# Kernel optimization log

Hardware: AMD Instinct MI355X
Metric: run time of the kernel (lower is better)

Reference implementation:

```python
import jax, jax.numpy as jnp
import numpy as np

NUM_HEADS = 16
HEAD_DIM = 64
D_DEC = 1024
D_ENC = 1024
R = 256  # kv_lora_rank
LN_EPS = 1e-5


def setup_inputs() -> dict:
    key = jax.random.key(0)
    ks = jax.random.split(key, 8)
    B, SQ, SK = 4, 2048, 4096
    query = jax.random.normal(ks[0], (B, SQ, D_DEC), dtype=jnp.float32)
    encoder_output = jax.random.normal(ks[1], (B, SK, D_ENC), dtype=jnp.float32)
    s = 0.02
    Wq = jax.random.normal(ks[2], (NUM_HEADS * HEAD_DIM, D_DEC), dtype=jnp.float32) * s
    Wkva = jax.random.normal(ks[3], (R, D_ENC), dtype=jnp.float32) * s
    ln_g = jnp.ones((R,), dtype=jnp.float32)
    ln_b = jnp.zeros((R,), dtype=jnp.float32)
    Wkvb = jax.random.normal(ks[4], (NUM_HEADS * 2 * HEAD_DIM, R), dtype=jnp.float32) * s
    Wout = jax.random.normal(ks[5], (D_DEC, NUM_HEADS * HEAD_DIM), dtype=jnp.float32) * s
    return {"query": query, "encoder_output": encoder_output, "Wq": Wq,
            "Wkva": Wkva, "ln_g": ln_g, "ln_b": ln_b, "Wkvb": Wkvb, "Wout": Wout}


def reference(query, encoder_output, Wq, Wkva, ln_g, ln_b, Wkvb, Wout):
    B, SQ, _ = query.shape
    SK = encoder_output.shape[1]
    H, Dh = NUM_HEADS, HEAD_DIM

    # q projection -> [B, H, SQ, Dh]
    q = jnp.einsum('bsd,ed->bse', query, Wq).reshape(B, SQ, H, Dh).transpose(0, 2, 1, 3)

    # low-rank KV compression + layernorm
    c = jnp.einsum('bsd,rd->bsr', encoder_output, Wkva)  # [B, SK, R]
    mu = jnp.mean(c, axis=-1, keepdims=True)
    var = jnp.mean(jnp.square(c - mu), axis=-1, keepdims=True)
    c = (c - mu) * jax.lax.rsqrt(var + LN_EPS) * ln_g + ln_b

    # decompress to K,V: [B, SK, H, 2*Dh] -> split
    kv = jnp.einsum('bsr,er->bse', c, Wkvb).reshape(B, SK, H, 2 * Dh).transpose(0, 2, 1, 3)
    k, v = kv[..., :Dh], kv[..., Dh:]

    scale = 1.0 / np.sqrt(Dh).astype(np.float32)
    scores = jnp.einsum('bhqd,bhkd->bhqk', q, k) * scale
    attn = jax.nn.softmax(scores, axis=-1)  # dropout is identity in eval / p=0
    o = jnp.einsum('bhqk,bhkd->bhqd', attn, v)
    o = o.transpose(0, 2, 1, 3).reshape(B, SQ, H * Dh)
    return jnp.einsum('bse,de->bsd', o, Wout)
```

## Files before the change

### kernel.cpp

```cpp
#include <hip/hip_runtime.h>

#define LOG2E 1.4426950408889634f

typedef __attribute__((ext_vector_type(8))) short short8;
typedef __attribute__((ext_vector_type(4))) float f32x4;
typedef __attribute__((ext_vector_type(16))) float f32x16;
typedef __attribute__((ext_vector_type(4))) unsigned u32x4;

__device__ inline unsigned short f2bf(float f) {
  unsigned u = __float_as_uint(f);
  u += 0x7fffu + ((u >> 16) & 1u);
  return (unsigned short)(u >> 16);
}

#define MFMA16(a, b, c) __builtin_amdgcn_mfma_f32_16x16x32_bf16((a), (b), (c), 0, 0, 0)
#define MFMA32(a, b, c) __builtin_amdgcn_mfma_f32_32x32x16_bf16((a), (b), (c), 0, 0, 0)

#define GLDS16(gp, lp)                                                              \
  __builtin_amdgcn_global_load_lds((const __attribute__((address_space(1))) void*)(gp), \
                                   (__attribute__((address_space(3))) void*)(lp), 16, 0, 0)

__device__ inline f32x4 zero4() {
  f32x4 z = {0.f, 0.f, 0.f, 0.f};
  return z;
}
__device__ inline f32x16 zero16() {
  f32x16 z = {0.f, 0.f, 0.f, 0.f, 0.f, 0.f, 0.f, 0.f, 0.f, 0.f, 0.f, 0.f, 0.f, 0.f, 0.f, 0.f};
  return z;
}
__device__ inline unsigned cvtpk_bf16(float a, float b) {
  unsigned r;
  asm("v_cvt_pk_bf16_f32 %0, %1, %2" : "=v"(r) : "v"(a), "v"(b));
  return r;
}
__device__ inline void plswap(unsigned& a, unsigned& b) {
  asm("v_permlane32_swap_b32 %0, %1" : "+v"(a), "+v"(b));
}

__global__ __launch_bounds__(256) void k_cast6(
    const float* __restrict__ e, const float* __restrict__ q, const float* __restrict__ wq,
    const float* __restrict__ wo, const float* __restrict__ wb, const float* __restrict__ wa,
    unsigned short* __restrict__ eo, unsigned short* __restrict__ qo, unsigned short* __restrict__ wqo,
    unsigned short* __restrict__ woo, unsigned short* __restrict__ wbo, unsigned short* __restrict__ wao) {
  int i = (blockIdx.x * 256 + threadIdx.x) * 4;
  const float* src;
  unsigned short* dst;
  int off;
  if (i < 16777216) { src = e; dst = eo; off = i; }
  else if (i < 25165824) { src = q; dst = qo; off = i - 16777216; }
  else if (i < 26214400) { src = wq; dst = wqo; off = i - 25165824; }
  else if (i < 27262976) { src = wo; dst = woo; off = i - 26214400; }
  else if (i < 27787264) { src = wb; dst = wbo; off = i - 27262976; }
  else { src = wa; dst = wao; off = i - 27787264; }
  float4 v = *(const float4*)(src + off);
  unsigned lo = (unsigned)f2bf(v.x) | ((unsigned)f2bf(v.y) << 16);
  unsigned hi = (unsigned)f2bf(v.z) | ((unsigned)f2bf(v.w) << 16);
  *(uint2*)(dst + off) = make_uint2(lo, hi);
}

__global__ __launch_bounds__(256, 2) void k_qproj(const unsigned short* __restrict__ A,
                                                  const unsigned short* __restrict__ Bw,
                                                  unsigned short* __restrict__ Qout) {
  __shared__ __align__(16) short As[128 * 32];
  __shared__ __align__(16) short Bs[128 * 32];
  const int K = 1024;
  int tid = threadIdx.x;
  int w = tid >> 6, lane = tid & 63, quad = lane >> 4, c = lane & 15;
  int m0 = blockIdx.x * 128, n0 = blockIdx.y * 128;
  int wm = (w >> 1) * 64, wn = (w & 1) * 64;
  f32x4 acc[4][4];
#pragma unroll
  for (int i = 0; i < 4; i++)
#pragma unroll
    for (int j = 0; j < 4; j++) acc[i][j] = zero4();

  for (int k0 = 0; k0 < K; k0 += 32) {
#pragma unroll
    for (int i = 0; i < 2; i++) {
      int seg = w * 2 + i;
      int bo = seg * 1024 + lane * 16;
      int row = bo >> 6, col = (bo & 63) >> 1;
      GLDS16(A + (size_t)(m0 + row) * K + k0 + col, (char*)As + seg * 1024);
      GLDS16(Bw + (size_t)(n0 + row) * K + k0 + col, (char*)Bs + seg * 1024);
    }
    __syncthreads();
    short8 af[4], bfr[4];
#pragma unroll
    for (int i = 0; i < 4; i++) {
      af[i] = *(const short8*)&As[(wm + i * 16 + c) * 32 + quad * 8];
      bfr[i] = *(const short8*)&Bs[(wn + i * 16 + c) * 32 + quad * 8];
    }
#pragma unroll
    for (int mi = 0; mi < 4; mi++)
#pragma unroll
      for (int ni = 0; ni < 4; ni++) acc[mi][ni] = MFMA16(af[mi], bfr[ni], acc[mi][ni]);
    __syncthreads();
  }
  const float scale = 0.125f * LOG2E;
#pragma unroll
  for (int mi = 0; mi < 4; mi++) {
    int rowb = m0 + wm + mi * 16 + quad * 4;
#pragma unroll
    for (int ni = 0; ni < 4; ni++) {
      int col = n0 + wn + ni * 16 + c;
      int h = col >> 6, d = col & 63;
#pragma unroll
      for (int r = 0; r < 4; r++) {
        int row = rowb + r;
        int b = row >> 11, sq = row & 2047;
        Qout[(((size_t)(b * 16 + h)) * 2048 + sq) * 64 + d] = f2bf(acc[mi][ni][r] * scale);
      }
    }
  }
}

__global__ __launch_bounds__(256, 2) void k_cln(const unsigned short* __restrict__ E,
                                                const unsigned short* __restrict__ Wa,
                                                const float* __restrict__ g, const float* __restrict__ bb,
                                                unsigned short* __restrict__ Cout) {
  __shared__ __align__(16) short As[64 * 32];
  __shared__ __align__(16) short Bs[256 * 32];
  __shared__ float redS[4][64], redQ[4][64];
  __shared__ float gS[256], bS[256];
  const int K = 1024;
  int tid = threadIdx.x;
  int w = tid >> 6, lane = tid & 63, quad = lane >> 4, c = lane & 15;
  int m0 = blockIdx.x * 64;
  gS[tid] = g[tid];
  bS[tid] = bb[tid];
  f32x4 acc[4][4];
#pragma unroll
  for (int i = 0; i < 4; i++)
#pragma unroll
    for (int j = 0; j < 4; j++) acc[i][j] = zero4();

  for (int k0 = 0; k0 < K; k0 += 32) {
    {
      int bo = w * 1024 + lane * 16;
      int row = bo >> 6, col = (bo & 63) >> 1;
      GLDS16(E + (size_t)(m0 + row) * K + k0 + col, (char*)As + w * 1024);
    }
#pragma unroll
    for (int i = 0; i < 4; i++) {
      int seg = w * 4 + i;
      int bo = seg * 1024 + lane * 16;
      int row = bo >> 6, col = (bo & 63) >> 1;
      GLDS16(Wa + (size_t)row * K + k0 + col, (char*)Bs + seg * 1024);
    }
    __syncthreads();
    short8 af[4], bfr[4];
#pragma unroll
    for (int i = 0; i < 4; i++) {
      af[i] = *(const short8*)&As[(i * 16 + c) * 32 + quad * 8];
      bfr[i] = *(const short8*)&Bs[(w * 64 + i * 16 + c) * 32 + quad * 8];
    }
#pragma unroll
    for (int mi = 0; mi < 4; mi++)
#pragma unroll
      for (int ni = 0; ni < 4; ni++) acc[mi][ni] = MFMA16(af[mi], bfr[ni], acc[mi][ni]);
    __syncthreads();
  }
  float ps[4][4], pq[4][4];
#pragma unroll
  for (int mi = 0; mi < 4; mi++)
#pragma unroll
    for (int r = 0; r < 4; r++) {
      float s = 0.f, q = 0.f;
#pragma unroll
      for (int ni = 0; ni < 4; ni++) {
        float x = acc[mi][ni][r];
        s += x;
        q += x * x;
      }
      for (int m = 1; m < 16; m <<= 1) {
        s += __shfl_xor(s, m, 64);
        q += __shfl_xor(q, m, 64);
      }
      ps[mi][r] = s;
      pq[mi][r] = q;
    }
  if (c == 0) {
#pragma unroll
    for (int mi = 0; mi < 4; mi++)
#pragma unroll
      for (int r = 0; r < 4; r++) {
        int row = mi * 16 + quad * 4 + r;
        redS[w][row] = ps[mi][r];
        redQ[w][row] = pq[mi][r];
      }
  }
  __syncthreads();
  float muv[4][4], rsv[4][4];
#pragma unroll
  for (int mi = 0; mi < 4; mi++)
#pragma unroll
    for (int r = 0; r < 4; r++) {
      int row = mi * 16 + quad * 4 + r;
      float S = redS[0][row] + redS[1][row] + redS[2][row] + redS[3][row];
      float Q = redQ[0][row] + redQ[1][row] + redQ[2][row] + redQ[3][row];
      float mu = S * (1.f / 256.f);
      float var = Q * (1.f / 256.f) - mu * mu;
      muv[mi][r] = mu;
      rsv[mi][r] = rsqrtf(var + 1e-5f);
    }
#pragma unroll
  for (int mi = 0; mi < 4; mi++)
#pragma unroll
    for (int ni = 0; ni < 4; ni++) {
      int col = w * 64 + ni * 16 + c;
#pragma unroll
      for (int r = 0; r < 4; r++) {
        int row = m0 + mi * 16 + quad * 4 + r;
        float y = (acc[mi][ni][r] - muv[mi][r]) * rsv[mi][r] * gS[col] + bS[col];
        Cout[(size_t)row * 256 + col] = f2bf(y);
      }
    }
}

__global__ __launch_bounds__(256, 2) void k_kv(const unsigned short* __restrict__ A,
                                               const unsigned short* __restrict__ Bw,
                                               unsigned short* __restrict__ Kb,
                                               unsigned short* __restrict__ Vb) {
  __shared__ __align__(16) short As[128 * 32];
  __shared__ __align__(16) short Bs[128 * 32];
  const int K = 256;
  int tid = threadIdx.x;
  int w = tid >> 6, lane = tid & 63, quad = lane >> 4, c = lane & 15;
  int m0 = blockIdx.x * 128, n0 = blockIdx.y * 128;
  int wm = (w >> 1) * 64, wn = (w & 1) * 64;
  f32x4 acc[4][4];
#pragma unroll
  for (int i = 0; i < 4; i++)
#pragma unroll
    for (int j = 0; j < 4; j++) acc[i][j] = zero4();

  for (int k0 = 0; k0 < K; k0 += 32) {
#pragma unroll
    for (int i = 0; i < 2; i++) {
      int seg = w * 2 + i;
      int bo = seg * 1024 + lane * 16;
      int row = bo >> 6, col = (bo & 63) >> 1;
      GLDS16(A + (size_t)(m0 + row) * K + k0 + col, (char*)As + seg * 1024);
      GLDS16(Bw + (size_t)(n0 + row) * K + k0 + col, (char*)Bs + seg * 1024);
    }
    __syncthreads();
    short8 af[4], bfr[4];
#pragma unroll
    for (int i = 0; i < 4; i++) {
      af[i] = *(const short8*)&As[(wm + i * 16 + c) * 32 + quad * 8];
      bfr[i] = *(const short8*)&Bs[(wn + i * 16 + c) * 32 + quad * 8];
    }
#pragma unroll
    for (int mi = 0; mi < 4; mi++)
#pragma unroll
      for (int ni = 0; ni < 4; ni++) acc[mi][ni] = MFMA16(af[mi], bfr[ni], acc[mi][ni]);
    __syncthreads();
  }
#pragma unroll
  for (int mi = 0; mi < 4; mi++) {
    int rowb = m0 + wm + mi * 16 + quad * 4;
#pragma unroll
    for (int ni = 0; ni < 4; ni++) {
      int col = n0 + wn + ni * 16 + c;
      int h = col >> 7, rr = col & 127;
#pragma unroll
      for (int r = 0; r < 4; r++) {
        int row = rowb + r;
        int b = row >> 12, sk = row & 4095;
        int kt = sk >> 6, ki = sk & 63;
        size_t base = ((size_t)(b * 16 + h)) * 262144 + (size_t)kt * 4096;
        float x = acc[mi][ni][r];
        if (rr < 64) {
          int d = rr;
          int half = ki >> 5, l31k = ki & 31, ds = d >> 4, dhi = (d >> 3) & 1, j = d & 7;
          Kb[base + (size_t)((half * 4 + ds) * 64 + l31k + 32 * dhi) * 8 + j] = f2bf(x);
        } else {
          int d = rr - 64;
          int dt = d >> 5, sg = ki >> 4, khi = (ki >> 3) & 1, j = ki & 7;
          Vb[base + (size_t)((dt * 4 + sg) * 64 + (d & 31) + 32 * khi) * 8 + j] = f2bf(x);
        }
      }
    }
  }
}

__device__ __forceinline__ void attn_tile(const char* Kl, const char* Vl,
                                          const short8 (&qf)[4], f32x16 (&O)[2], float& lp) {
#pragma unroll
  for (int h = 0; h < 2; h++) {
    short8 kf[4];
#pragma unroll
    for (int ds = 0; ds < 4; ds++) kf[ds] = *(const short8*)(Kl + (h * 4 + ds) * 1024);
    f32x16 S = zero16();
#pragma unroll
    for (int ds = 0; ds < 4; ds++) S = MFMA32(kf[ds], qf[ds], S);
    float lpa = 0.f, lpb = 0.f;
    unsigned u[8];
#pragma unroll
    for (int m = 0; m < 8; m++) {
      float p0 = __builtin_amdgcn_exp2f(S[2 * m]);
      float p1 = __builtin_amdgcn_exp2f(S[2 * m + 1]);
      if (m & 1) lpb += p0 + p1; else lpa += p0 + p1;
      u[m] = cvtpk_bf16(p0, p1);
    }
    lp += lpa + lpb;
    plswap(u[0], u[2]);
    plswap(u[1], u[3]);
    plswap(u[4], u[6]);
    plswap(u[5], u[7]);
    u32x4 w0 = {u[0], u[1], u[2], u[3]};
    u32x4 w1 = {u[4], u[5], u[6], u[7]};
    short8 paf0 = __builtin_bit_cast(short8, w0);
    short8 paf1 = __builtin_bit_cast(short8, w1);
#pragma unroll
    for (int dt = 0; dt < 2; dt++) {
      short8 vf0 = *(const short8*)(Vl + (dt * 4 + h * 2 + 0) * 1024);
      short8 vf1 = *(const short8*)(Vl + (dt * 4 + h * 2 + 1) * 1024);
      O[dt] = MFMA32(paf0, vf0, O[dt]);
      O[dt] = MFMA32(paf1, vf1, O[dt]);
    }
  }
}

__global__ __launch_bounds__(256, 4) void k_attn(const unsigned short* __restrict__ Qb,
                                                 const unsigned short* __restrict__ Kb,
                                                 const unsigned short* __restrict__ Vb,
                                                 unsigned short* __restrict__ Ob) {
  __shared__ __align__(16) short KA[8192];
  __shared__ __align__(16) short KB[8192];
  int tid = threadIdx.x;
  int w = tid >> 6, lane = tid & 63;
  int l31 = lane & 31, hi = lane >> 5;
  int qt = blockIdx.x, bh = blockIdx.y;

  const char* Kg = (const char*)Kb + (size_t)bh * 524288;
  const char* Vg = (const char*)Vb + (size_t)bh * 524288;
  int ldsseg = (w < 2) ? w * 4 : 8 + (w - 2) * 4;
  const char* sgbase = ((w < 2) ? Kg + (w * 4) * 1024 : Vg + ((w - 2) * 4) * 1024) + lane * 16;

  const unsigned short* Qrow = Qb + ((size_t)bh * 2048 + qt * 128 + w * 32 + l31) * 64 + hi * 8;
  short8 qf[4];
#pragma unroll
  for (int ds = 0; ds < 4; ds++) qf[ds] = *(const short8*)(Qrow + ds * 16);

  f32x16 O[2];
  float lp = 0.f;
#pragma unroll
  for (int j = 0; j < 2; j++) O[j] = zero16();

#pragma unroll
  for (int i = 0; i < 4; i++) GLDS16(sgbase + i * 1024, (char*)KA + (ldsseg + i) * 1024);
  sgbase += 8192;
  __syncthreads();

  for (int kt2 = 0; kt2 < 64; kt2 += 2) {
    {
#pragma unroll
      for (int i = 0; i < 4; i++)
        GLDS16(sgbase + i * 1024, (char*)KB + (ldsseg + i) * 1024);
      sgbase += 8192;
      attn_tile((const char*)KA + lane * 16, (const char*)KA + lane * 16 + 8192, qf, O, lp);
      __syncthreads();
    }
    {
      if (kt2 < 62) {
#pragma unroll
        for (int i = 0; i < 4; i++)
          GLDS16(sgbase + i * 1024, (char*)KA + (ldsseg + i) * 1024);
        sgbase += 8192;
      }
      attn_tile((const char*)KB + lane * 16, (const char*)KB + lane * 16 + 8192, qf, O, lp);
      __syncthreads();
    }
  }

  lp += __shfl_xor(lp, 32, 64);
  int b = bh >> 4, hh = bh & 15;
#pragma unroll
  for (int r = 0; r < 16; r++) {
    int qrow = (r & 3) + 8 * (r >> 2) + 4 * hi;
    float inv = __builtin_amdgcn_rcpf(__shfl(lp, qrow, 64));
    size_t orow = ((size_t)b * 2048 + qt * 128 + w * 32 + qrow) * 1024 + hh * 64 + l31;
    Ob[orow] = f2bf(O[0][r] * inv);
    Ob[orow + 32] = f2bf(O[1][r] * inv);
  }
}

__global__ __launch_bounds__(256, 2) void k_out(const unsigned short* __restrict__ A,
                                                const unsigned short* __restrict__ Bw,
                                                float* __restrict__ Out) {
  __shared__ __align__(16) short As[128 * 32];
  __shared__ __align__(16) short Bs[128 * 32];
  const int K = 1024;
  int tid = threadIdx.x;
  int w = tid >> 6, lane = tid & 63, quad = lane >> 4, c = lane & 15;
  int m0 = blockIdx.x * 128, n0 = blockIdx.y * 128;
  int wm = (w >> 1) * 64, wn = (w & 1) * 64;
  f32x4 acc[4][4];
#pragma unroll
  for (int i = 0; i < 4; i++)
#pragma unroll
    for (int j = 0; j < 4; j++) acc[i][j] = zero4();

  for (int k0 = 0; k0 < K; k0 += 32) {
#pragma unroll
    for (int i = 0; i < 2; i++) {
      int seg = w * 2 + i;
      int bo = seg * 1024 + lane * 16;
      int row = bo >> 6, col = (bo & 63) >> 1;
      GLDS16(A + (size_t)(m0 + row) * K + k0 + col, (char*)As + seg * 1024);
      GLDS16(Bw + (size_t)(n0 + row) * K + k0 + col, (char*)Bs + seg * 1024);
    }
    __syncthreads();
    short8 af[4], bfr[4];
#pragma unroll
    for (int i = 0; i < 4; i++) {
      af[i] = *(const short8*)&As[(wm + i * 16 + c) * 32 + quad * 8];
      bfr[i] = *(const short8*)&Bs[(wn + i * 16 + c) * 32 + quad * 8];
    }
#pragma unroll
    for (int mi = 0; mi < 4; mi++)
#pragma unroll
      for (int ni = 0; ni < 4; ni++) acc[mi][ni] = MFMA16(af[mi], bfr[ni], acc[mi][ni]);
    __syncthreads();
  }
#pragma unroll
  for (int mi = 0; mi < 4; mi++) {
    int rowb = m0 + wm + mi * 16 + quad * 4;
#pragma unroll
    for (int ni = 0; ni < 4; ni++) {
      int col = n0 + wn + ni * 16 + c;
#pragma unroll
      for (int r = 0; r < 4; r++) Out[(size_t)(rowb + r) * 1024 + col] = acc[mi][ni][r];
    }
  }
}

extern "C" void kernel_launch(void* const* d_in, const int* in_sizes, int n_in,
                              void* d_out, int out_size, void* d_ws, size_t ws_size,
                              hipStream_t stream) {
  const float* query = (const float*)d_in[0];
  const float* enc = (const float*)d_in[1];
  const float* Wq = (const float*)d_in[2];
  const float* Wkva = (const float*)d_in[3];
  const float* ln_g = (const float*)d_in[4];
  const float* ln_b = (const float*)d_in[5];
  const float* Wkvb = (const float*)d_in[6];
  const float* Wout = (const float*)d_in[7];
  if (ws_size < 81264640) return;

  char* ws = (char*)d_ws;
  unsigned short* wq_bf = (unsigned short*)(ws + 0);
  unsigned short* wa_bf = (unsigned short*)(ws + 2097152);
  unsigned short* wb_bf = (unsigned short*)(ws + 2621440);
  unsigned short* wo_bf = (unsigned short*)(ws + 3670016);
  unsigned short* qproj = (unsigned short*)(ws + 5767168);
  unsigned short* cln = (unsigned short*)(ws + 22544384);
  unsigned short* ebf_v = (unsigned short*)(ws + 30932992);
  unsigned short* qin_o = (unsigned short*)(ws + 64487424);
  unsigned short* kbuf = (unsigned short*)d_out;

  k_cast6<<<27392, 256, 0, stream>>>(enc, query, Wq, Wout, Wkvb, Wkva,
                                     ebf_v, qin_o, wq_bf, wo_bf, wb_bf, wa_bf);

  k_qproj<<<dim3(64, 8), 256, 0, stream>>>(qin_o, wq_bf, qproj);
  k_cln<<<256, 256, 0, stream>>>(ebf_v, wa_bf, ln_g, ln_b, cln);
  k_kv<<<dim3(128, 16), 256, 0, stream>>>(cln, wb_bf, kbuf, ebf_v);
  k_attn<<<dim3(16, 64), 256, 0, stream>>>(qproj, kbuf, ebf_v, qin_o);
  k_out<<<dim3(64, 8), 256, 0, stream>>>(qin_o, wo_bf, (float*)d_out);
}
```

Baseline: 423.2 us.

## Fuse activation bf16 casts into GEMM loaders, vectorize V stores, prioritize MFMA

The separate cast kernel no longer converts the large encoder and query activations. The q-projection and compression GEMMs now read fp32 directly, convert to bf16 in registers and store into LDS, which removes a full write and re-read of the bf16 copies. The K/V epilogue is restructured to pack four bf16 V values per 8-byte store. In the attention inner loop, setprio is raised around the MFMA groups. The trade-off is that the GEMM A loads become synchronous register loads instead of async global-to-LDS loads, so that latency is exposed.

```diff
diff --git a/kernel.cpp b/kernel.cpp
--- a/kernel.cpp
+++ b/kernel.cpp
@@ -37,28 +37,26 @@
   asm("v_permlane32_swap_b32 %0, %1" : "+v"(a), "+v"(b));
 }
 
-__global__ __launch_bounds__(256) void k_cast6(
-    const float* __restrict__ e, const float* __restrict__ q, const float* __restrict__ wq,
-    const float* __restrict__ wo, const float* __restrict__ wb, const float* __restrict__ wa,
-    unsigned short* __restrict__ eo, unsigned short* __restrict__ qo, unsigned short* __restrict__ wqo,
-    unsigned short* __restrict__ woo, unsigned short* __restrict__ wbo, unsigned short* __restrict__ wao) {
+__global__ __launch_bounds__(256) void k_cast4(
+    const float* __restrict__ wq, const float* __restrict__ wo,
+    const float* __restrict__ wb, const float* __restrict__ wa,
+    unsigned short* __restrict__ wqo, unsigned short* __restrict__ woo,
+    unsigned short* __restrict__ wbo, unsigned short* __restrict__ wao) {
   int i = (blockIdx.x * 256 + threadIdx.x) * 4;
   const float* src;
   unsigned short* dst;
   int off;
-  if (i < 16777216) { src = e; dst = eo; off = i; }
-  else if (i < 25165824) { src = q; dst = qo; off = i - 16777216; }
-  else if (i < 26214400) { src = wq; dst = wqo; off = i - 25165824; }
-  else if (i < 27262976) { src = wo; dst = woo; off = i - 26214400; }
-  else if (i < 27787264) { src = wb; dst = wbo; off = i - 27262976; }
-  else { src = wa; dst = wao; off = i - 27787264; }
+  if (i < 1048576) { src = wq; dst = wqo; off = i; }
+  else if (i < 2097152) { src = wo; dst = woo; off = i - 1048576; }
+  else if (i < 2621440) { src = wb; dst = wbo; off = i - 2097152; }
+  else { src = wa; dst = wao; off = i - 2621440; }
   float4 v = *(const float4*)(src + off);
   unsigned lo = (unsigned)f2bf(v.x) | ((unsigned)f2bf(v.y) << 16);
   unsigned hi = (unsigned)f2bf(v.z) | ((unsigned)f2bf(v.w) << 16);
   *(uint2*)(dst + off) = make_uint2(lo, hi);
 }
 
-__global__ __launch_bounds__(256, 2) void k_qproj(const unsigned short* __restrict__ A,
+__global__ __launch_bounds__(256, 2) void k_qproj(const float* __restrict__ A,
                                                   const unsigned short* __restrict__ Bw,
                                                   unsigned short* __restrict__ Qout) {
   __shared__ __align__(16) short As[128 * 32];
@@ -68,6 +66,7 @@
   int w = tid >> 6, lane = tid & 63, quad = lane >> 4, c = lane & 15;
   int m0 = blockIdx.x * 128, n0 = blockIdx.y * 128;
   int wm = (w >> 1) * 64, wn = (w & 1) * 64;
+  int rsub = lane >> 2, csub = (lane & 3) * 8;
   f32x4 acc[4][4];
 #pragma unroll
   for (int i = 0; i < 4; i++)
@@ -75,12 +74,21 @@
     for (int j = 0; j < 4; j++) acc[i][j] = zero4();
 
   for (int k0 = 0; k0 < K; k0 += 32) {
+#pragma unroll
+    for (int i = 0; i < 2; i++) {
+      int seg = w * 2 + i;
+      const float* Ap = A + (size_t)(m0 + seg * 16 + rsub) * K + k0 + csub;
+      float4 va = *(const float4*)Ap;
+      float4 vb2 = *(const float4*)(Ap + 4);
+      u32x4 pk = {cvtpk_bf16(va.x, va.y), cvtpk_bf16(va.z, va.w),
+                  cvtpk_bf16(vb2.x, vb2.y), cvtpk_bf16(vb2.z, vb2.w)};
+      *(u32x4*)((char*)As + seg * 1024 + lane * 16) = pk;
+    }
 #pragma unroll
     for (int i = 0; i < 2; i++) {
       int seg = w * 2 + i;
       int bo = seg * 1024 + lane * 16;
       int row = bo >> 6, col = (bo & 63) >> 1;
-      GLDS16(A + (size_t)(m0 + row) * K + k0 + col, (char*)As + seg * 1024);
       GLDS16(Bw + (size_t)(n0 + row) * K + k0 + col, (char*)Bs + seg * 1024);
     }
     __syncthreads();
@@ -114,7 +122,7 @@
   }
 }
 
-__global__ __launch_bounds__(256, 2) void k_cln(const unsigned short* __restrict__ E,
+__global__ __launch_bounds__(256, 2) void k_cln(const float* __restrict__ E,
                                                 const unsigned short* __restrict__ Wa,
                                                 const float* __restrict__ g, const float* __restrict__ bb,
                                                 unsigned short* __restrict__ Cout) {
@@ -126,6 +134,7 @@
   int tid = threadIdx.x;
   int w = tid >> 6, lane = tid & 63, quad = lane >> 4, c = lane & 15;
   int m0 = blockIdx.x * 64;
+  int rsub = lane >> 2, csub = (lane & 3) * 8;
   gS[tid] = g[tid];
   bS[tid] = bb[tid];
   f32x4 acc[4][4];
@@ -136,9 +145,12 @@
 
   for (int k0 = 0; k0 < K; k0 += 32) {
     {
-      int bo = w * 1024 + lane * 16;
-      int row = bo >> 6, col = (bo & 63) >> 1;
-      GLDS16(E + (size_t)(m0 + row) * K + k0 + col, (char*)As + w * 1024);
+      const float* Ep = E + (size_t)(m0 + w * 16 + rsub) * K + k0 + csub;
+      float4 va = *(const float4*)Ep;
+      float4 vb2 = *(const float4*)(Ep + 4);
+      u32x4 pk = {cvtpk_bf16(va.x, va.y), cvtpk_bf16(va.z, va.w),
+                  cvtpk_bf16(vb2.x, vb2.y), cvtpk_bf16(vb2.z, vb2.w)};
+      *(u32x4*)((char*)As + w * 1024 + lane * 16) = pk;
     }
 #pragma unroll
     for (int i = 0; i < 4; i++) {
@@ -259,26 +271,33 @@
 #pragma unroll
   for (int mi = 0; mi < 4; mi++) {
     int rowb = m0 + wm + mi * 16 + quad * 4;
+    int b = rowb >> 12;
+    int sk0 = rowb & 4095;
+    int kt = sk0 >> 6, ki0 = sk0 & 63;
+    int sg = ((wm + mi * 16) & 63) >> 4;
+    int khi = quad >> 1;
+    int j0 = (quad & 1) * 4;
 #pragma unroll
     for (int ni = 0; ni < 4; ni++) {
       int col = n0 + wn + ni * 16 + c;
       int h = col >> 7, rr = col & 127;
-#pragma unroll
-      for (int r = 0; r < 4; r++) {
-        int row = rowb + r;
-        int b = row >> 12, sk = row & 4095;
-        int kt = sk >> 6, ki = sk & 63;
-        size_t base = ((size_t)(b * 16 + h)) * 262144 + (size_t)kt * 4096;
-        float x = acc[mi][ni][r];
-        if (rr < 64) {
-          int d = rr;
-          int half = ki >> 5, l31k = ki & 31, ds = d >> 4, dhi = (d >> 3) & 1, j = d & 7;
-          Kb[base + (size_t)((half * 4 + ds) * 64 + l31k + 32 * dhi) * 8 + j] = f2bf(x);
-        } else {
-          int d = rr - 64;
-          int dt = d >> 5, sg = ki >> 4, khi = (ki >> 3) & 1, j = ki & 7;
-          Vb[base + (size_t)((dt * 4 + sg) * 64 + (d & 31) + 32 * khi) * 8 + j] = f2bf(x);
+      size_t base = ((size_t)(b * 16 + h)) * 262144 + (size_t)kt * 4096;
+      if (rr < 64) {
+        int d = rr;
+        int ds = d >> 4, dhi = (d >> 3) & 1, j = d & 7;
+#pragma unroll
+        for (int r = 0; r < 4; r++) {
+          int ki = ki0 + r;
+          int half = ki >> 5, l31k = ki & 31;
+          Kb[base + (size_t)((half * 4 + ds) * 64 + l31k + 32 * dhi) * 8 + j] = f2bf(acc[mi][ni][r]);
         }
+      } else {
+        int d = rr - 64;
+        int dt = d >> 5;
+        unsigned lo = (unsigned)f2bf(acc[mi][ni][0]) | ((unsigned)f2bf(acc[mi][ni][1]) << 16);
+        unsigned hi = (unsigned)f2bf(acc[mi][ni][2]) | ((unsigned)f2bf(acc[mi][ni][3]) << 16);
+        *(uint2*)(Vb + base + (size_t)((dt * 4 + sg) * 64 + (d & 31) + 32 * khi) * 8 + j0) =
+            make_uint2(lo, hi);
       }
     }
   }
@@ -292,8 +311,10 @@
 #pragma unroll
     for (int ds = 0; ds < 4; ds++) kf[ds] = *(const short8*)(Kl + (h * 4 + ds) * 1024);
     f32x16 S = zero16();
+    __builtin_amdgcn_s_setprio(1);
 #pragma unroll
     for (int ds = 0; ds < 4; ds++) S = MFMA32(kf[ds], qf[ds], S);
+    __builtin_amdgcn_s_setprio(0);
     float lpa = 0.f, lpb = 0.f;
     unsigned u[8];
 #pragma unroll
@@ -312,6 +333,7 @@
     u32x4 w1 = {u[4], u[5], u[6], u[7]};
     short8 paf0 = __builtin_bit_cast(short8, w0);
     short8 paf1 = __builtin_bit_cast(short8, w1);
+    __builtin_amdgcn_s_setprio(1);
 #pragma unroll
     for (int dt = 0; dt < 2; dt++) {
       short8 vf0 = *(const short8*)(Vl + (dt * 4 + h * 2 + 0) * 1024);
@@ -319,6 +341,7 @@
       O[dt] = MFMA32(paf0, vf0, O[dt]);
       O[dt] = MFMA32(paf1, vf1, O[dt]);
     }
+    __builtin_amdgcn_s_setprio(0);
   }
 }
 
@@ -456,16 +479,15 @@
   unsigned short* wo_bf = (unsigned short*)(ws + 3670016);
   unsigned short* qproj = (unsigned short*)(ws + 5767168);
   unsigned short* cln = (unsigned short*)(ws + 22544384);
-  unsigned short* ebf_v = (unsigned short*)(ws + 30932992);
-  unsigned short* qin_o = (unsigned short*)(ws + 64487424);
+  unsigned short* vbuf = (unsigned short*)(ws + 30932992);
+  unsigned short* obuf = (unsigned short*)(ws + 64487424);
   unsigned short* kbuf = (unsigned short*)d_out;
 
-  k_cast6<<<27392, 256, 0, stream>>>(enc, query, Wq, Wout, Wkvb, Wkva,
-                                     ebf_v, qin_o, wq_bf, wo_bf, wb_bf, wa_bf);
-
-  k_qproj<<<dim3(64, 8), 256, 0, stream>>>(qin_o, wq_bf, qproj);
-  k_cln<<<256, 256, 0, stream>>>(ebf_v, wa_bf, ln_g, ln_b, cln);
-  k_kv<<<dim3(128, 16), 256, 0, stream>>>(cln, wb_bf, kbuf, ebf_v);
-  k_attn<<<dim3(16, 64), 256, 0, stream>>>(qproj, kbuf, ebf_v, qin_o);
-  k_out<<<dim3(64, 8), 256, 0, stream>>>(qin_o, wo_bf, (float*)d_out);
-}
+  k_cast4<<<2816, 256, 0, stream>>>(Wq, Wout, Wkvb, Wkva, wq_bf, wo_bf, wb_bf, wa_bf);
+
+  k_qproj<<<dim3(64, 8), 256, 0, stream>>>(query, wq_bf, qproj);
+  k_cln<<<256, 256, 0, stream>>>(enc, wa_bf, ln_g, ln_b, cln);
+  k_kv<<<dim3(128, 16), 256, 0, stream>>>(cln, wb_bf, kbuf, vbuf);
+  k_attn<<<dim3(16, 64), 256, 0, stream>>>(qproj, kbuf, vbuf, obuf);
+  k_out<<<dim3(64, 8), 256, 0, stream>>>(obuf, wo_bf, (float*)d_out);
+}
```

Result: slower. 455.9 us (+7.7%).
